# Optimization experiments

Hardware: AMD Instinct MI355X
Metric: run time of the kernel (lower is better)

Reference implementation:

```python
import jax, jax.numpy as jnp
import numpy as np

NUM_HEADS = 12
EPS = 1e-6


def setup_inputs() -> dict:
    key = jax.random.key(0)
    k1, k2, k3, k4, k5 = jax.random.split(key, 5)
    B, N, C = 8, 4096, 768
    scale = 1.0 / np.sqrt(C)
    return {
        "x": jax.random.normal(k1, (B, N, C), dtype=jnp.float32),
        "W_qkv": jax.random.normal(k2, (C, 3 * C), dtype=jnp.float32) * scale,
        "b_qkv": jax.random.normal(k3, (3 * C,), dtype=jnp.float32) * 0.02,
        "W_proj": jax.random.normal(k4, (C, C), dtype=jnp.float32) * scale,
        "b_proj": jax.random.normal(k5, (C,), dtype=jnp.float32) * 0.02,
    }


def reference(x, W_qkv, b_qkv, W_proj, b_proj):
    B, N, C = x.shape
    H = NUM_HEADS
    D = C // H
    # qkv projection -> (3, B, H, N, D)
    qkv = (x @ W_qkv + b_qkv).reshape(B, N, 3, H, D).transpose(2, 0, 3, 1, 4)
    q, k, v = qkv[0], qkv[1], qkv[2]
    q = jax.nn.sigmoid(q)
    k = jax.nn.sigmoid(k)
    ksum = k.sum(axis=2)  # [B,H,D]
    qsum = q.sum(axis=2)  # [B,H,D]
    # incoming/outgoing flow normalizers, [B,H,N]
    sink_incoming = 1.0 / (jnp.einsum('bhnd,bhd->bhn', q + EPS, ksum + EPS) + EPS)
    source_outgoing = 1.0 / (jnp.einsum('bhnd,bhd->bhn', k + EPS, qsum + EPS) + EPS)
    conserved_sink = jnp.einsum(
        'bhnd,bhd->bhn', q + EPS, (k * source_outgoing[..., None]).sum(axis=2) + EPS) + EPS
    conserved_source = jnp.einsum(
        'bhnd,bhd->bhn', k + EPS, (q * sink_incoming[..., None]).sum(axis=2) + EPS) + EPS
    conserved_source = jnp.clip(conserved_source, -1.0, 1.0)
    sink_allocation = jax.nn.sigmoid(conserved_sink * (float(N) / float(N)))
    source_competition = jax.nn.softmax(conserved_source, axis=-1) * float(N)
    # linear attention: kv = k^T @ (v * competition), [B,H,D,D]
    kv = jnp.einsum('bhnd,bhne->bhde', k, v * source_competition[..., None])
    x_update = jnp.einsum('bhnd,bhde->bhne', q, kv)
    x_update = x_update * sink_incoming[..., None] * sink_allocation[..., None]
    out = x_update.transpose(0, 2, 1, 3).reshape(B, N, C)
    out = out @ W_proj + b_proj
    return jax.nn.sigmoid(2.0 * out)
```

## Files before the change

kernel.cpp:

```cpp
#include <hip/hip_runtime.h>
#include <stdint.h>

#define EPSF 1e-6f

typedef unsigned short u16;
typedef __attribute__((ext_vector_type(8))) short short8;
typedef __attribute__((ext_vector_type(4))) float f32x4;

__device__ __forceinline__ float us2f(u16 u) {
  union { float f; unsigned int i; } c; c.i = ((unsigned int)u) << 16; return c.f;
}
__device__ __forceinline__ u16 f2bfu(float f) {
  union { float f; unsigned int i; } c; c.f = f;
  unsigned int i = c.i;
  return (u16)((i + 0x7FFFu + ((i >> 16) & 1u)) >> 16);
}
__device__ __forceinline__ float sigm(float x) { return 1.f / (1.f + __expf(-x)); }

typedef __attribute__((address_space(3))) unsigned int lds_u32;
typedef const __attribute__((address_space(1))) unsigned int glb_u32;
__device__ __forceinline__ void gl_lds16(const u16* g, u16* l) {
  __builtin_amdgcn_global_load_lds((glb_u32*)g, (lds_u32*)l, 16, 0, 0);
}

__global__ void k_cvt_x(const float* __restrict__ in, u16* __restrict__ out) {
  const int i = blockIdx.x * 256 + threadIdx.x;
  float4 v = ((const float4*)in)[i];
  ushort4 o;
  o.x = f2bfu(v.x); o.y = f2bfu(v.y); o.z = f2bfu(v.z); o.w = f2bfu(v.w);
  ((ushort4*)out)[i] = o;
}

__global__ void k_transpose(const float* __restrict__ in, u16* __restrict__ out, int R, int C) {
  __shared__ float tile[32][33];
  const int tx = threadIdx.x & 31, ty = threadIdx.x >> 5;
  const int c0 = blockIdx.x << 5, r0 = blockIdx.y << 5;
  for (int i = ty; i < 32; i += 8) tile[i][tx] = in[(size_t)(r0 + i) * C + c0 + tx];
  __syncthreads();
  for (int i = ty; i < 32; i += 8) out[(size_t)(c0 + i) * R + r0 + tx] = f2bfu(tile[tx][i]);
}

template <int MODE>
__global__ __launch_bounds__(512, 2) void k_gemm(
    const u16* __restrict__ A, const u16* __restrict__ BT,
    const float* __restrict__ bias,
    u16* __restrict__ qkvo, float* __restrict__ qsum, float* __restrict__ ksum,
    float* __restrict__ outf)
{
  __shared__ __align__(16) u16 smem[65536];
  const int tid = threadIdx.x;
  const int lane = tid & 63;
  const int wid = tid >> 6;
  const int wm = wid >> 2, wn = wid & 3;
  const int nx = gridDim.x;
  int lid = blockIdx.y * nx + blockIdx.x;
  const int q8 = (nx * gridDim.y) >> 3;
  lid = (lid & 7) * q8 + (lid >> 3);
  const int m0 = (lid / nx) << 8;
  const int n0 = (lid % nx) << 8;

  const int rowS = tid >> 2;
  const int sub  = tid & 3;
  const int subx = sub ^ ((rowS >> 1) & 3);
  const u16* gA = A  + (size_t)(m0 + rowS) * 768 + (subx << 3);
  const u16* gB = BT + (size_t)(n0 + rowS) * 768 + (subx << 3);
  const int dstc = tid << 3;

  const int r16 = lane & 15;
  const int sgrp = lane >> 4;
  int offA[8], offB[4];
#pragma unroll
  for (int mi = 0; mi < 8; ++mi) {
    const int ra = (wm << 7) + (mi << 4) + r16;
    offA[mi] = ra * 32 + ((sgrp ^ ((ra >> 1) & 3)) << 3);
  }
#pragma unroll
  for (int nj = 0; nj < 4; ++nj) {
    const int rb = (wn << 6) + (nj << 4) + r16;
    offB[nj] = rb * 32 + ((sgrp ^ ((rb >> 1) & 3)) << 3);
  }

  f32x4 acc[8][4];
#pragma unroll
  for (int i = 0; i < 8; ++i)
#pragma unroll
    for (int j = 0; j < 4; ++j) acc[i][j] = (f32x4){0.f, 0.f, 0.f, 0.f};

#define STAGE(kh)                                                   \
  do {                                                              \
    const int khs = ((kh) > 23 ? 23 : (kh)) << 5;                   \
    const int so = ((kh) & 3) << 13;                                \
    gl_lds16(gA + khs,         &smem[so + dstc]);                   \
    gl_lds16(gA + 98304 + khs, &smem[so + dstc + 4096]);            \
    gl_lds16(gB + khs,         &smem[32768 + so + dstc]);           \
    gl_lds16(gB + 98304 + khs, &smem[32768 + so + dstc + 4096]);    \
  } while (0)

  STAGE(0); STAGE(1); STAGE(2);

  for (int kh = 0; kh < 24; ++kh) {
    asm volatile("s_waitcnt vmcnt(8)" ::: "memory");
    __builtin_amdgcn_s_barrier();
    __builtin_amdgcn_sched_barrier(0);
    STAGE(kh + 3);
    const u16* pa = &smem[(kh & 3) << 13];
    const u16* pb = pa + 32768;
    short8 bf[4];
#pragma unroll
    for (int nj = 0; nj < 4; ++nj) bf[nj] = *(const short8*)(pb + offB[nj]);
    __builtin_amdgcn_s_setprio(1);
#pragma unroll
    for (int mi = 0; mi < 8; ++mi) {
      const short8 av = *(const short8*)(pa + offA[mi]);
#pragma unroll
      for (int nj = 0; nj < 4; ++nj)
        acc[mi][nj] = __builtin_amdgcn_mfma_f32_16x16x32_bf16(av, bf[nj], acc[mi][nj], 0, 0, 0);
    }
    __builtin_amdgcn_s_setprio(0);
  }
#undef STAGE
  asm volatile("s_waitcnt vmcnt(0)" ::: "memory");

  if (MODE == 0) {
    const int colc = n0 + (wn << 6);
    const bool sg = (colc < 1536);
    float jsum[4] = {0.f, 0.f, 0.f, 0.f};
#pragma unroll
    for (int mi = 0; mi < 8; ++mi) {
      const int rowb = m0 + (wm << 7) + (mi << 4) + ((lane >> 4) << 2);
#pragma unroll
      for (int nj = 0; nj < 4; ++nj) {
        const int col = colc + (nj << 4) + r16;
        const float bcol = bias[col];
        if (sg) {
#pragma unroll
          for (int rg = 0; rg < 4; ++rg) {
            const float val = sigm(acc[mi][nj][rg] + bcol);
            jsum[nj] += val;
            qkvo[(size_t)(rowb + rg) * 2304 + col] = f2bfu(val);
          }
        } else {
#pragma unroll
          for (int rg = 0; rg < 4; ++rg)
            qkvo[(size_t)(rowb + rg) * 2304 + col] = f2bfu(acc[mi][nj][rg] + bcol);
        }
      }
    }
    if (sg) {
#pragma unroll
      for (int nj = 0; nj < 4; ++nj) {
        jsum[nj] += __shfl_xor(jsum[nj], 16, 64);
        jsum[nj] += __shfl_xor(jsum[nj], 32, 64);
      }
      if (lane < 16) {
        const int b12 = (m0 >> 12) * 12;
        float* sdst = (colc >= 768) ? ksum : qsum;
        const int cb = (colc >= 768) ? colc - 768 : colc;
#pragma unroll
        for (int nj = 0; nj < 4; ++nj)
          atomicAdd(&sdst[(b12 << 6) + cb + (nj << 4) + r16], jsum[nj]);
      }
    }
  } else {
#pragma unroll
    for (int mi = 0; mi < 8; ++mi) {
      const int rowb = m0 + (wm << 7) + (mi << 4) + ((lane >> 4) << 2);
#pragma unroll
      for (int nj = 0; nj < 4; ++nj) {
        const int col = n0 + (wn << 6) + (nj << 4) + r16;
        const float bcol = bias[col];
#pragma unroll
        for (int rg = 0; rg < 4; ++rg)
          outf[(size_t)(rowb + rg) * 768 + col] = sigm(2.f * (acc[mi][nj][rg] + bcol));
      }
    }
  }
}

__global__ __launch_bounds__(256) void k_flow1(
    const u16* __restrict__ qkv,
    const float* __restrict__ qsum, const float* __restrict__ ksum,
    float* __restrict__ si_out, float* __restrict__ qsi, float* __restrict__ kso)
{
  const int bh = blockIdx.x >> 3, sp = blockIdx.x & 7;
  const int lane = threadIdx.x & 63, wid = threadIdx.x >> 6;
  const int j = lane & 15;
  const int grp = (wid << 2) | (lane >> 4);
  const u16* base = qkv + (size_t)(bh / 12) * 4096 * 2304 + (bh % 12) * 64;
  float ke[4], qe[4];
#pragma unroll
  for (int t = 0; t < 4; ++t) {
    ke[t] = ksum[(bh << 6) + (j << 2) + t] + EPSF;
    qe[t] = qsum[(bh << 6) + (j << 2) + t] + EPSF;
  }
  float Sk = ke[0] + ke[1] + ke[2] + ke[3];
  float Sq = qe[0] + qe[1] + qe[2] + qe[3];
#pragma unroll
  for (int msk = 1; msk < 16; msk <<= 1) { Sk += __shfl_xor(Sk, msk, 64); Sq += __shfl_xor(Sq, msk, 64); }
  const float cK = EPSF * Sk + EPSF;
  const float cQ = EPSF * Sq + EPSF;
  float aq0 = 0, aq1 = 0, aq2 = 0, aq3 = 0, ak0 = 0, ak1 = 0, ak2 = 0, ak3 = 0;
  const int nbase = sp << 9;
  for (int it = 0; it < 32; ++it) {
    const int n = nbase + (it << 4) + grp;
    const size_t ro = (size_t)n * 2304 + (j << 2);
    const uint64_t lq = *(const uint64_t*)(base + ro);
    const uint64_t lk = *(const uint64_t*)(base + ro + 768);
    const float q0 = us2f((u16)lq), q1 = us2f((u16)(lq >> 16)), q2 = us2f((u16)(lq >> 32)), q3 = us2f((u16)(lq >> 48));
    const float k0 = us2f((u16)lk), k1 = us2f((u16)(lk >> 16)), k2 = us2f((u16)(lk >> 32)), k3 = us2f((u16)(lk >> 48));
    float dq = q0 * ke[0] + q1 * ke[1] + q2 * ke[2] + q3 * ke[3];
    float dk = k0 * qe[0] + k1 * qe[1] + k2 * qe[2] + k3 * qe[3];
#pragma unroll
    for (int msk = 1; msk < 16; msk <<= 1) { dq += __shfl_xor(dq, msk, 64); dk += __shfl_xor(dk, msk, 64); }
    const float si = 1.f / (dq + cK);
    const float so = 1.f / (dk + cQ);
    if (j == 0) si_out[(bh << 12) + n] = si;
    aq0 += q0 * si; aq1 += q1 * si; aq2 += q2 * si; aq3 += q3 * si;
    ak0 += k0 * so; ak1 += k1 * so; ak2 += k2 * so; ak3 += k3 * so;
  }
  __shared__ float redq[16][64];
  __shared__ float redk[16][64];
  redq[grp][(j << 2) + 0] = aq0; redq[grp][(j << 2) + 1] = aq1;
  redq[grp][(j << 2) + 2] = aq2; redq[grp][(j << 2) + 3] = aq3;
  redk[grp][(j << 2) + 0] = ak0; redk[grp][(j << 2) + 1] = ak1;
  redk[grp][(j << 2) + 2] = ak2; redk[grp][(j << 2) + 3] = ak3;
  __syncthreads();
  if (threadIdx.x < 64) {
    float s1 = 0.f, s2 = 0.f;
#pragma unroll
    for (int g = 0; g < 16; ++g) { s1 += redq[g][threadIdx.x]; s2 += redk[g][threadIdx.x]; }
    atomicAdd(&qsi[(bh << 6) + threadIdx.x], s1);
    atomicAdd(&kso[(bh << 6) + threadIdx.x], s2);
  }
}

__global__ __launch_bounds__(256) void k_fkv(
    const u16* __restrict__ qkv,
    const float* __restrict__ qsi, const float* __restrict__ kso,
    const float* __restrict__ si_in,
    float* __restrict__ mo, float* __restrict__ sumexp, float* __restrict__ kvm)
{
  __shared__ __align__(16) u16 smem[2 * 64 * 136];
  u16* kT = smem;
  u16* vT = smem + 64 * 136;
  const int tid = threadIdx.x;
  const int bh = blockIdx.x >> 3, sp = blockIdx.x & 7;
  const int lane = tid & 63, wid = tid >> 6;
  const int r16 = lane & 15, g = lane >> 4;
  const u16* base = qkv + (size_t)(bh / 12) * 4096 * 2304 + (bh % 12) * 64;
  const float* sib = si_in + ((size_t)bh << 12);
  float* mob = mo + ((size_t)bh << 12);

  const int d0 = (tid & 7) << 3;
  float qie[8], soe[8];
#pragma unroll
  for (int u = 0; u < 8; ++u) {
    qie[u] = qsi[(bh << 6) + d0 + u] + EPSF;
    soe[u] = kso[(bh << 6) + d0 + u] + EPSF;
  }
  float Sq = qsi[(bh << 6) + lane] + EPSF;
  float Sk = kso[(bh << 6) + lane] + EPSF;
#pragma unroll
  for (int m = 1; m < 64; m <<= 1) { Sq += __shfl_xor(Sq, m, 64); Sk += __shfl_xor(Sk, m, 64); }
  const float cR = EPSF * Sq + EPSF;
  const float cS = EPSF * Sk + EPSF;

  f32x4 acc[4][4];
#pragma unroll
  for (int i = 0; i < 4; ++i)
#pragma unroll
    for (int j = 0; j < 4; ++j) acc[i][j] = (f32x4){0.f, 0.f, 0.f, 0.f};

  const int nf = (wid << 5) + (g << 3);
  float esum = 0.f;

  for (int st = 0; st < 4; ++st) {
    const int nst = (sp << 9) + (st << 7);
#pragma unroll
    for (int i = 0; i < 4; ++i) {
      const int c = tid + (i << 8);
      const int nl = c >> 3;
      const int ng = nst + nl;
      const u16* rp = base + (size_t)ng * 2304 + d0;
      short8 q8 = *(const short8*)(rp);
      short8 k8 = *(const short8*)(rp + 768);
      short8 v8 = *(const short8*)(rp + 1536);
      float pcs = 0.f, pcr = 0.f;
#pragma unroll
      for (int u = 0; u < 8; ++u) {
        pcs += us2f((u16)q8[u]) * soe[u];
        pcr += us2f((u16)k8[u]) * qie[u];
      }
#pragma unroll
      for (int m = 1; m < 8; m <<= 1) { pcs += __shfl_xor(pcs, m, 64); pcr += __shfl_xor(pcr, m, 64); }
      float cr = pcr + cR;
      cr = fminf(1.f, fmaxf(-1.f, cr));
      const float ev = __expf(cr);
      const int col = nl ^ (d0 & 56);
#pragma unroll
      for (int u = 0; u < 8; ++u) {
        kT[(d0 + u) * 136 + col] = f2bfu(us2f((u16)k8[u]) * ev);
        vT[(d0 + u) * 136 + col] = (u16)(unsigned short)v8[u];
      }
      if ((tid & 7) == 0) {
        mob[ng] = sib[ng] * sigm(pcs + cS);
        esum += ev;
      }
    }
    __syncthreads();

    short8 af[4], bf[4];
#pragma unroll
    for (int mi = 0; mi < 4; ++mi) {
      const int row = (mi << 4) + r16;
      af[mi] = *(const short8*)&kT[row * 136 + (nf ^ (row & 56))];
    }
#pragma unroll
    for (int nj = 0; nj < 4; ++nj) {
      const int row = (nj << 4) + r16;
      bf[nj] = *(const short8*)&vT[row * 136 + (nf ^ (row & 56))];
    }
#pragma unroll
    for (int mi = 0; mi < 4; ++mi)
#pragma unroll
      for (int nj = 0; nj < 4; ++nj)
        acc[mi][nj] = __builtin_amdgcn_mfma_f32_16x16x32_bf16(af[mi], bf[nj], acc[mi][nj], 0, 0, 0);
    __syncthreads();
  }

  float* red = (float*)smem;
  float* kvb = kvm + ((size_t)bh << 12);
#pragma unroll
  for (int half = 0; half < 2; ++half) {
#pragma unroll
    for (int m2 = 0; m2 < 2; ++m2) {
      const int mi = (half << 1) + m2;
#pragma unroll
      for (int nj = 0; nj < 4; ++nj)
#pragma unroll
        for (int rg = 0; rg < 4; ++rg)
          red[(wid << 11) + (((m2 << 4) + (g << 2) + rg) << 6) + (nj << 4) + r16] = acc[mi][nj][rg];
    }
    __syncthreads();
    const int base2 = tid << 3;
#pragma unroll
    for (int u2 = 0; u2 < 2; ++u2) {
      const int o = base2 + (u2 << 2);
      float4 s0 = *(const float4*)&red[o];
      float4 s1 = *(const float4*)&red[2048 + o];
      float4 s2 = *(const float4*)&red[4096 + o];
      float4 s3 = *(const float4*)&red[6144 + o];
      s0.x += s1.x + s2.x + s3.x;
      s0.y += s1.y + s2.y + s3.y;
      s0.z += s1.z + s2.z + s3.z;
      s0.w += s1.w + s2.w + s3.w;
      const int gi = (half << 11) + o;
      atomicAdd(&kvb[gi + 0], s0.x);
      atomicAdd(&kvb[gi + 1], s0.y);
      atomicAdd(&kvb[gi + 2], s0.z);
      atomicAdd(&kvb[gi + 3], s0.w);
    }
    __syncthreads();
  }

  esum += __shfl_xor(esum, 8, 64);
  esum += __shfl_xor(esum, 16, 64);
  esum += __shfl_xor(esum, 32, 64);
  if (lane == 0) atomicAdd(&sumexp[bh], esum);
}

__global__ __launch_bounds__(256) void k_xup(
    const u16* __restrict__ qkv, const float* __restrict__ kvm,
    const float* __restrict__ m_arr, const float* __restrict__ sumexp,
    u16* __restrict__ attn)
{
  const int bh = blockIdx.y;
  const int n0 = blockIdx.x << 7;
  const int b = bh / 12, h = bh % 12;
  __shared__ __align__(16) u16 qs[128 * 72];
  __shared__ __align__(16) u16 kvs[64 * 72];
  const int tid = threadIdx.x, lane = tid & 63, wid = tid >> 6;
  const u16* qg = qkv + (size_t)b * 4096 * 2304 + (size_t)n0 * 2304 + h * 64;
#pragma unroll
  for (int i = 0; i < 4; ++i) {
    const int c = tid + (i << 8);
    const int nl = c >> 3, d0 = (c & 7) << 3;
    *(short8*)&qs[nl * 72 + d0] = *(const short8*)(qg + (size_t)nl * 2304 + d0);
  }
  const float* kvg = kvm + ((size_t)bh << 12);
#pragma unroll
  for (int i = 0; i < 4; ++i) {
    const int idx = (tid << 2) + (i << 10);
    const int d = idx >> 6, e0 = idx & 63;
    float4 vv = *(const float4*)(kvg + idx);
    kvs[(e0 + 0) * 72 + d] = f2bfu(vv.x);
    kvs[(e0 + 1) * 72 + d] = f2bfu(vv.y);
    kvs[(e0 + 2) * 72 + d] = f2bfu(vv.z);
    kvs[(e0 + 3) * 72 + d] = f2bfu(vv.w);
  }
  __syncthreads();
  const float scale = 4096.f / sumexp[bh];
  const int r16 = lane & 15, kg8 = (lane >> 4) << 3;
  f32x4 acc[2][4];
#pragma unroll
  for (int i = 0; i < 2; ++i)
#pragma unroll
    for (int j = 0; j < 4; ++j) acc[i][j] = (f32x4){0.f, 0.f, 0.f, 0.f};
#pragma unroll
  for (int kk = 0; kk < 2; ++kk) {
    short8 af[2], bfv[4];
#pragma unroll
    for (int mi = 0; mi < 2; ++mi)
      af[mi] = *(const short8*)&qs[((wid << 5) + (mi << 4) + r16) * 72 + (kk << 5) + kg8];
#pragma unroll
    for (int nj = 0; nj < 4; ++nj)
      bfv[nj] = *(const short8*)&kvs[((nj << 4) + r16) * 72 + (kk << 5) + kg8];
#pragma unroll
    for (int mi = 0; mi < 2; ++mi)
#pragma unroll
      for (int nj = 0; nj < 4; ++nj)
        acc[mi][nj] = __builtin_amdgcn_mfma_f32_16x16x32_bf16(af[mi], bfv[nj], acc[mi][nj], 0, 0, 0);
  }
#pragma unroll
  for (int mi = 0; mi < 2; ++mi) {
#pragma unroll
    for (int rg = 0; rg < 4; ++rg) {
      const int n = n0 + (wid << 5) + (mi << 4) + ((lane >> 4) << 2) + rg;
      const float mult = m_arr[((size_t)bh << 12) + n] * scale;
#pragma unroll
      for (int nj = 0; nj < 4; ++nj) {
        const int e = (nj << 4) + r16;
        attn[((size_t)(b * 4096 + n)) * 768 + (h << 6) + e] = f2bfu(acc[mi][nj][rg] * mult);
      }
    }
  }
}

extern "C" void kernel_launch(void* const* d_in, const int* in_sizes, int n_in,
                              void* d_out, int out_size, void* d_ws, size_t ws_size,
                              hipStream_t stream)
{
  (void)in_sizes; (void)n_in; (void)out_size; (void)ws_size;
  const float* x     = (const float*)d_in[0];
  const float* Wqkv  = (const float*)d_in[1];
  const float* bqkv  = (const float*)d_in[2];
  const float* Wproj = (const float*)d_in[3];
  const float* bproj = (const float*)d_in[4];
  float* out = (float*)d_out;

  char* ws = (char*)d_ws;
  size_t off = 0;
  auto alloc = [&](size_t bytes) -> char* {
    char* p = ws + off;
    off += (bytes + 255) & ~(size_t)255;
    return p;
  };
  u16* qkv  = (u16*)alloc(150994944);
  u16* xbf  = (u16*)alloc(50331648);
  u16* WqT  = (u16*)alloc(3538944);
  u16* WpT  = (u16*)alloc(1179648);
  float* si = (float*)alloc(1572864);
  float* mb = (float*)alloc(1572864);
  char* zbase = ws + off;
  float* qsum   = (float*)alloc(24576);
  float* ksum   = (float*)alloc(24576);
  float* qsi    = (float*)alloc(24576);
  float* kso    = (float*)alloc(24576);
  float* sumexp = (float*)alloc(512);
  float* kvm    = (float*)alloc(1572864);
  const size_t zbytes = (size_t)((ws + off) - zbase);

  hipMemsetAsync(zbase, 0, zbytes, stream);
  k_cvt_x<<<24576, 256, 0, stream>>>(x, xbf);
  k_transpose<<<dim3(72, 24), 256, 0, stream>>>(Wqkv, WqT, 768, 2304);
  k_transpose<<<dim3(24, 24), 256, 0, stream>>>(Wproj, WpT, 768, 768);
  k_gemm<0><<<dim3(9, 128), 512, 0, stream>>>(xbf, WqT, bqkv, qkv, qsum, ksum, nullptr);
  k_flow1<<<768, 256, 0, stream>>>(qkv, qsum, ksum, si, qsi, kso);
  k_fkv<<<768, 256, 0, stream>>>(qkv, qsi, kso, si, mb, sumexp, kvm);
  k_xup<<<dim3(32, 96), 256, 0, stream>>>(qkv, kvm, mb, sumexp, xbf);
  k_gemm<1><<<dim3(3, 128), 512, 0, stream>>>(xbf, WpT, bproj, nullptr, nullptr, nullptr, out);
}
```

Measured before the change: 416.8 us.

## Split GEMM K-step into four interleaved load/MFMA phases with barriers

Restructures the GEMM main loop so each K-step runs as four phases. Each phase issues one global-to-LDS load, reads two A fragments from LDS, then runs eight MFMAs. This spreads the memory instructions among the matrix ops, in the style of a ping-pong schedule, so load issue and LDS reads overlap with compute. It adds many more s_barrier calls per iteration, which can stall waves if they fall out of step.

New measurement: 422.0 us. Within noise of the previous version (+1.3%).

```diff
diff --git a/kernel.cpp b/kernel.cpp
--- a/kernel.cpp
+++ b/kernel.cpp
@@ -86,39 +86,94 @@
 #pragma unroll
     for (int j = 0; j < 4; ++j) acc[i][j] = (f32x4){0.f, 0.f, 0.f, 0.f};
 
-#define STAGE(kh)                                                   \
-  do {                                                              \
-    const int khs = ((kh) > 23 ? 23 : (kh)) << 5;                   \
-    const int so = ((kh) & 3) << 13;                                \
-    gl_lds16(gA + khs,         &smem[so + dstc]);                   \
-    gl_lds16(gA + 98304 + khs, &smem[so + dstc + 4096]);            \
-    gl_lds16(gB + khs,         &smem[32768 + so + dstc]);           \
-    gl_lds16(gB + 98304 + khs, &smem[32768 + so + dstc + 4096]);    \
+#define STAGE1(kh, c)                                                 \
+  do {                                                                \
+    const int khs = ((kh) > 23 ? 23 : (kh)) << 5;                     \
+    const int so = ((kh) & 3) << 13;                                  \
+    if ((c) == 0)      gl_lds16(gA + khs,          &smem[so + dstc]);             \
+    else if ((c) == 1) gl_lds16(gA + 98304 + khs,  &smem[so + dstc + 4096]);      \
+    else if ((c) == 2) gl_lds16(gB + khs,          &smem[32768 + so + dstc]);     \
+    else               gl_lds16(gB + 98304 + khs,  &smem[32768 + so + dstc + 4096]); \
   } while (0)
 
-  STAGE(0); STAGE(1); STAGE(2);
+#pragma unroll
+  for (int t = 0; t < 3; ++t) {
+    STAGE1(t, 0); STAGE1(t, 1); STAGE1(t, 2); STAGE1(t, 3);
+  }
+  asm volatile("s_waitcnt vmcnt(8)" ::: "memory");
+  __builtin_amdgcn_s_barrier();
+
+#define MFMA8(P, X0, X1)                                                                  \
+  do {                                                                                    \
+    acc[2*(P)][0] = __builtin_amdgcn_mfma_f32_16x16x32_bf16((X0), b0, acc[2*(P)][0], 0, 0, 0); \
+    acc[2*(P)][1] = __builtin_amdgcn_mfma_f32_16x16x32_bf16((X0), b1, acc[2*(P)][1], 0, 0, 0); \
+    acc[2*(P)][2] = __builtin_amdgcn_mfma_f32_16x16x32_bf16((X0), b2, acc[2*(P)][2], 0, 0, 0); \
+    acc[2*(P)][3] = __builtin_amdgcn_mfma_f32_16x16x32_bf16((X0), b3, acc[2*(P)][3], 0, 0, 0); \
+    acc[2*(P)+1][0] = __builtin_amdgcn_mfma_f32_16x16x32_bf16((X1), b0, acc[2*(P)+1][0], 0, 0, 0); \
+    acc[2*(P)+1][1] = __builtin_amdgcn_mfma_f32_16x16x32_bf16((X1), b1, acc[2*(P)+1][1], 0, 0, 0); \
+    acc[2*(P)+1][2] = __builtin_amdgcn_mfma_f32_16x16x32_bf16((X1), b2, acc[2*(P)+1][2], 0, 0, 0); \
+    acc[2*(P)+1][3] = __builtin_amdgcn_mfma_f32_16x16x32_bf16((X1), b3, acc[2*(P)+1][3], 0, 0, 0); \
+  } while (0)
 
   for (int kh = 0; kh < 24; ++kh) {
-    asm volatile("s_waitcnt vmcnt(8)" ::: "memory");
-    __builtin_amdgcn_s_barrier();
-    __builtin_amdgcn_sched_barrier(0);
-    STAGE(kh + 3);
     const u16* pa = &smem[(kh & 3) << 13];
     const u16* pb = pa + 32768;
-    short8 bf[4];
-#pragma unroll
-    for (int nj = 0; nj < 4; ++nj) bf[nj] = *(const short8*)(pb + offB[nj]);
+
+    short8 b0 = *(const short8*)(pb + offB[0]);
+    short8 b1 = *(const short8*)(pb + offB[1]);
+    short8 b2 = *(const short8*)(pb + offB[2]);
+    short8 b3 = *(const short8*)(pb + offB[3]);
+    short8 a0 = *(const short8*)(pa + offA[0]);
+    short8 a1 = *(const short8*)(pa + offA[1]);
+    STAGE1(kh + 3, 0);
+    __builtin_amdgcn_s_barrier();
+    asm volatile("s_waitcnt lgkmcnt(0)" ::: "memory");
+    __builtin_amdgcn_sched_barrier(0);
     __builtin_amdgcn_s_setprio(1);
-#pragma unroll
-    for (int mi = 0; mi < 8; ++mi) {
-      const short8 av = *(const short8*)(pa + offA[mi]);
-#pragma unroll
-      for (int nj = 0; nj < 4; ++nj)
-        acc[mi][nj] = __builtin_amdgcn_mfma_f32_16x16x32_bf16(av, bf[nj], acc[mi][nj], 0, 0, 0);
-    }
+    MFMA8(0, a0, a1);
     __builtin_amdgcn_s_setprio(0);
-  }
-#undef STAGE
+    __builtin_amdgcn_sched_barrier(0);
+    __builtin_amdgcn_s_barrier();
+
+    a0 = *(const short8*)(pa + offA[2]);
+    a1 = *(const short8*)(pa + offA[3]);
+    STAGE1(kh + 3, 1);
+    __builtin_amdgcn_s_barrier();
+    asm volatile("s_waitcnt lgkmcnt(0)" ::: "memory");
+    __builtin_amdgcn_sched_barrier(0);
+    __builtin_amdgcn_s_setprio(1);
+    MFMA8(1, a0, a1);
+    __builtin_amdgcn_s_setprio(0);
+    __builtin_amdgcn_sched_barrier(0);
+    __builtin_amdgcn_s_barrier();
+
+    a0 = *(const short8*)(pa + offA[4]);
+    a1 = *(const short8*)(pa + offA[5]);
+    STAGE1(kh + 3, 2);
+    __builtin_amdgcn_s_barrier();
+    asm volatile("s_waitcnt lgkmcnt(0)" ::: "memory");
+    __builtin_amdgcn_sched_barrier(0);
+    __builtin_amdgcn_s_setprio(1);
+    MFMA8(2, a0, a1);
+    __builtin_amdgcn_s_setprio(0);
+    __builtin_amdgcn_sched_barrier(0);
+    __builtin_amdgcn_s_barrier();
+
+    a0 = *(const short8*)(pa + offA[6]);
+    a1 = *(const short8*)(pa + offA[7]);
+    STAGE1(kh + 3, 3);
+    __builtin_amdgcn_s_barrier();
+    asm volatile("s_waitcnt lgkmcnt(0)" ::: "memory");
+    __builtin_amdgcn_sched_barrier(0);
+    __builtin_amdgcn_s_setprio(1);
+    MFMA8(3, a0, a1);
+    __builtin_amdgcn_s_setprio(0);
+    __builtin_amdgcn_sched_barrier(0);
+    asm volatile("s_waitcnt vmcnt(8)" ::: "memory");
+    __builtin_amdgcn_s_barrier();
+  }
+#undef MFMA8
+#undef STAGE1
   asm volatile("s_waitcnt vmcnt(0)" ::: "memory");
 
   if (MODE == 0) {
```
